# Kernel optimization log

Hardware: AMD Instinct MI355X
Metric: run time of the kernel (lower is better)

Reference implementation:

```python
import jax, jax.numpy as jnp
import numpy as np

B, S, HID = 1, 2048, 2048
NH, NKV, D = 32, 4, 128   # query heads, kv heads, head_dim
ROPE_THETA = 1e6
EPS = 1e-6


def _rms_norm(x, w):
    # per-head RMSNorm over head_dim, computed in fp32 (Qwen3MoeRMSNorm)
    xf = x.astype(jnp.float32)
    var = jnp.mean(xf * xf, axis=-1, keepdims=True)
    return (w * (xf * jax.lax.rsqrt(var + EPS))).astype(x.dtype)


def _rotate_half(x):
    x1, x2 = jnp.split(x, 2, axis=-1)
    return jnp.concatenate([-x2, x1], axis=-1)


def setup_inputs() -> dict:
    key = jax.random.key(0)
    ks = jax.random.split(key, 5)
    hidden_states = jax.random.normal(ks[0], (B, S, HID), jnp.float32)
    # weights stored as (in, out); torch Linear computes x @ W.T with W (out,in) -- same math
    wq = jax.random.normal(ks[1], (HID, NH * D), jnp.float32) * 0.02
    wk = jax.random.normal(ks[2], (HID, NKV * D), jnp.float32) * 0.02
    wv = jax.random.normal(ks[3], (HID, NKV * D), jnp.float32) * 0.02
    wo = jax.random.normal(ks[4], (NH * D, HID), jnp.float32) * 0.02
    q_norm_w = jnp.ones((D,), jnp.float32)
    k_norm_w = jnp.ones((D,), jnp.float32)
    # RoPE tables (rotate_half convention, like HF Qwen3)
    inv_freq = 1.0 / (ROPE_THETA ** (jnp.arange(0, D, 2, dtype=jnp.float32) / D))
    freqs = jnp.arange(S, dtype=jnp.float32)[:, None] * inv_freq[None, :]  # [S, D/2]
    emb = jnp.concatenate([freqs, freqs], axis=-1)  # [S, D]
    cos, sin = jnp.cos(emb), jnp.sin(emb)
    # causal mask (True = keep)
    attention_mask = jnp.tril(jnp.ones((S, S), bool))[None, None]
    return {
        'hidden_states': hidden_states, 'cos': cos, 'sin': sin,
        'wq': wq, 'wk': wk, 'wv': wv, 'wo': wo,
        'q_norm_w': q_norm_w, 'k_norm_w': k_norm_w,
        'attention_mask': attention_mask, 'start_pos': 0,
    }


def reference(hidden_states, cos, sin, wq, wk, wv, wo, q_norm_w, k_norm_w,
              attention_mask, start_pos):
    b, s, _ = hidden_states.shape
    # projections + per-head RMSNorm, then [B, H, S, D]
    q = _rms_norm((hidden_states @ wq).reshape(b, s, NH, D), q_norm_w).transpose(0, 2, 1, 3)
    k = _rms_norm((hidden_states @ wk).reshape(b, s, NKV, D), k_norm_w).transpose(0, 2, 1, 3)
    v = (hidden_states @ wv).reshape(b, s, NKV, D).transpose(0, 2, 1, 3)
    # rotary embedding (rotate_half form); start_pos=0 -> tables already aligned
    c = cos[None, None, :, :]
    sn = sin[None, None, :, :]
    q = q * c + _rotate_half(q) * sn
    k = k * c + _rotate_half(k) * sn
    # GQA: repeat kv heads to match query heads
    groups = NH // NKV
    k = jnp.repeat(k, groups, axis=1)
    v = jnp.repeat(v, groups, axis=1)
    scaling = D ** -0.5
    scores = jnp.einsum('bhqd,bhkd->bhqk', q, k) * scaling  # [B, NH, S, S]
    scores = jnp.where(attention_mask, scores, jnp.float32(-1e9))
    attn = jax.nn.softmax(scores, axis=-1)
    out = jnp.einsum('bhqk,bhkd->bhqd', attn, v)  # [B, NH, S, D]
    out = out.transpose(0, 2, 1, 3).reshape(b, s, NH * D)
    return out @ wo
```

## Files before the change

### kernel.cpp

```cpp
#include <hip/hip_runtime.h>
#include <hip/hip_bf16.h>

using short4v = __attribute__((ext_vector_type(4))) short;
using short8 = __attribute__((ext_vector_type(8))) short;
using f32x4  = __attribute__((ext_vector_type(4))) float;

#define SEQ 2048
#define NHEAD 32
#define NKVH 4
#define HDIM 128
#define QK_SCALE_LOG2 (0.08838834764831845f * 1.44269504088896340f)

__device__ __forceinline__ float fast_exp2(float x) { return __builtin_amdgcn_exp2f(x); }
__device__ __forceinline__ float b2f(short u) {
    return __uint_as_float(((unsigned)(unsigned short)u) << 16);
}
__device__ __forceinline__ short f2bb(float f) {
    __hip_bfloat16 h = __float2bfloat16(f);
    return *reinterpret_cast<short*>(&h);
}

__global__ __launch_bounds__(256) void prep_kernel(
    const float* __restrict__ hs, __hip_bfloat16* __restrict__ hsb,
    const float* __restrict__ wq, const float* __restrict__ wk, const float* __restrict__ wv,
    const float* __restrict__ wo,
    __hip_bfloat16* __restrict__ WqkvT, __hip_bfloat16* __restrict__ WoT) {
    const int b = blockIdx.x, tid = threadIdx.x;
    if (b < 4096) {
        int i = b * 256 + tid;
        float4 v = ((const float4*)hs)[i];
        __hip_bfloat16 h4[4] = {__float2bfloat16(v.x), __float2bfloat16(v.y),
                                __float2bfloat16(v.z), __float2bfloat16(v.w)};
        ((ushort4*)hsb)[i] = *(ushort4*)h4;
        return;
    }
    __shared__ float tile[32][33];
    const float* W; __hip_bfloat16* Wt; int N, ld, nb, kb;
    if (b < 12288)      { int bb = b - 4096;  W = wq; Wt = WqkvT;                       N = 4096; ld = 2048; nb = (bb & 127) * 32; kb = (bb >> 7) * 32; }
    else if (b < 13312) { int bb = b - 12288; W = wk; Wt = WqkvT + (size_t)4096 * 2048; N = 512;  ld = 2048; nb = (bb & 15) * 32;  kb = (bb >> 4) * 32; }
    else if (b < 14336) { int bb = b - 13312; W = wv; Wt = WqkvT + (size_t)4608 * 2048; N = 512;  ld = 2048; nb = (bb & 15) * 32;  kb = (bb >> 4) * 32; }
    else                { int bb = b - 14336; W = wo; Wt = WoT;                         N = 2048; ld = 4096; nb = (bb & 63) * 32;  kb = (bb >> 6) * 32; }
    int tx = tid & 31, ty = tid >> 5;
    for (int j = 0; j < 32; j += 8)
        tile[ty + j][tx] = W[(size_t)(kb + ty + j) * N + nb + tx];
    __syncthreads();
    for (int j = 0; j < 32; j += 8)
        Wt[(size_t)(nb + ty + j) * ld + kb + tx] = __float2bfloat16(tile[tx][ty + j]);
}

__global__ void add3b_kernel(const __hip_bfloat16* __restrict__ a, const __hip_bfloat16* __restrict__ b,
                             const __hip_bfloat16* __restrict__ c, float* __restrict__ o, int n4) {
    int i = blockIdx.x * blockDim.x + threadIdx.x;
    if (i >= n4) return;
    short4v x = ((const short4v*)a)[i];
    short4v y = ((const short4v*)b)[i];
    short4v z = ((const short4v*)c)[i];
    float4 r = {b2f(x[0]) + b2f(y[0]) + b2f(z[0]), b2f(x[1]) + b2f(y[1]) + b2f(z[1]),
                b2f(x[2]) + b2f(y[2]) + b2f(z[2]), b2f(x[3]) + b2f(y[3]) + b2f(z[3])};
    ((float4*)o)[i] = r;
}

#define BM 128
#define BN 128
#define BKK 32
template <typename OutT>
__global__ __launch_bounds__(256) void gemm_bt_kernel(
    const __hip_bfloat16* __restrict__ A, const __hip_bfloat16* __restrict__ Bt,
    OutT* __restrict__ C, int M, int N, int KextMax, int ld, int koff, long long czstride, int Ktot) {
    const int kstart = blockIdx.z * koff;
    const int Kext = min(KextMax, Ktot - kstart);
    A  += (size_t)kstart;
    Bt += (size_t)kstart;
    C  += (size_t)blockIdx.z * czstride;
    __shared__ __align__(16) __hip_bfloat16 sA[BM * BKK];
    __shared__ __align__(16) __hip_bfloat16 sB[BN * BKK];
    const int tid = threadIdx.x;
    const int w = tid >> 6, l = tid & 63;
    const int wr = w >> 1, wc = w & 1;
    const int row0 = blockIdx.y * BM;
    const int col0 = blockIdx.x * BN;
    const int srow = l >> 2;
    const int scol = (l & 3) * 8;

    f32x4 acc[4][4] = {};
    const int fr = l & 15;
    const int fc = (l >> 4) * 8;

    for (int k0 = 0; k0 < Kext; k0 += BKK) {
        for (int i = 0; i < 2; ++i) {
            int c = i * 4 + w;
            const __hip_bfloat16* ga = A + (size_t)(row0 + c * 16 + srow) * ld + k0 + scol;
            __builtin_amdgcn_global_load_lds((const __attribute__((address_space(1))) void*)ga,
                                             (__attribute__((address_space(3))) void*)&sA[c * 16 * BKK], 16, 0, 0);
            const __hip_bfloat16* gb = Bt + (size_t)(col0 + c * 16 + srow) * ld + k0 + scol;
            __builtin_amdgcn_global_load_lds((const __attribute__((address_space(1))) void*)gb,
                                             (__attribute__((address_space(3))) void*)&sB[c * 16 * BKK], 16, 0, 0);
        }
        __syncthreads();
        short8 af[4], bfr[4];
        for (int m = 0; m < 4; ++m)
            af[m] = *(const short8*)&sA[(wr * 64 + m * 16 + fr) * BKK + fc];
        for (int n = 0; n < 4; ++n)
            bfr[n] = *(const short8*)&sB[(wc * 64 + n * 16 + fr) * BKK + fc];
        for (int m = 0; m < 4; ++m)
            for (int n = 0; n < 4; ++n)
                acc[m][n] = __builtin_amdgcn_mfma_f32_16x16x32_bf16(af[m], bfr[n], acc[m][n], 0, 0, 0);
        __syncthreads();
    }
    const int fq = l >> 4;
    for (int m = 0; m < 4; ++m)
        for (int n = 0; n < 4; ++n)
            for (int r = 0; r < 4; ++r) {
                int row = row0 + wr * 64 + m * 16 + fq * 4 + r;
                int col = col0 + wc * 64 + n * 16 + fr;
                float v = acc[m][n][r];
                if constexpr (__is_same(OutT, float)) C[(size_t)row * N + col] = v;
                else C[(size_t)row * N + col] = __float2bfloat16(v);
            }
}

__global__ __launch_bounds__(256) void pack_kernel(
    const __hip_bfloat16* __restrict__ P0, const __hip_bfloat16* __restrict__ P1,
    const float* __restrict__ cosp, const float* __restrict__ sinp,
    const float* __restrict__ qnw, const float* __restrict__ knw,
    __hip_bfloat16* __restrict__ Qh, __hip_bfloat16* __restrict__ Kh, __hip_bfloat16* __restrict__ Vt) {
    const int tid = threadIdx.x;
    const int rloc = tid >> 4, l16 = tid & 15;
    const int r = blockIdx.y * 16 + rloc;
    const int s = blockIdx.x * 2 + (r >= 40 ? 1 : 0);
    const int slot = (r >= 40) ? r - 40 : r;
    int off;
    if (slot < 32)      off = slot * 128;
    else if (slot < 36) off = 4096 + (slot - 32) * 128;
    else                off = 4608 + (slot - 36) * 128;
    const int d0 = l16 * 4;
    const size_t base = (size_t)s * 5120 + off;

    short4v a0 = *(const short4v*)&P0[base + d0];
    short4v a1 = *(const short4v*)&P0[base + d0 + 64];
    short4v b0 = *(const short4v*)&P1[base + d0];
    short4v b1 = *(const short4v*)&P1[base + d0 + 64];
    float x1[4], x2[4];
    for (int j = 0; j < 4; ++j) {
        x1[j] = b2f(a0[j]) + b2f(b0[j]);
        x2[j] = b2f(a1[j]) + b2f(b1[j]);
    }

    if (slot >= 36) {
        int t = slot - 36;
        for (int j = 0; j < 4; ++j) {
            Vt[((size_t)t * 128 + d0 + j) * SEQ + s]      = __float2bfloat16(x1[j]);
            Vt[((size_t)t * 128 + d0 + 64 + j) * SEQ + s] = __float2bfloat16(x2[j]);
        }
        return;
    }
    float ss = 0.f;
    for (int j = 0; j < 4; ++j) ss += x1[j] * x1[j] + x2[j] * x2[j];
    for (int x = 1; x < 16; x <<= 1) ss += __shfl_xor(ss, x);
    float rs = rsqrtf(ss * (1.0f / 128.0f) + 1e-6f);

    f32x4 c4 = *(const f32x4*)&cosp[(size_t)s * 128 + d0];
    f32x4 s4 = *(const f32x4*)&sinp[(size_t)s * 128 + d0];
    const float* wgt = (slot < 32) ? qnw : knw;
    f32x4 w1 = *(const f32x4*)&wgt[d0];
    f32x4 w2 = *(const f32x4*)&wgt[d0 + 64];
    const float scl = (slot < 32) ? QK_SCALE_LOG2 : 1.0f;

    short4v o1, o2;
    for (int j = 0; j < 4; ++j) {
        float a = x1[j] * rs * w1[j], b = x2[j] * rs * w2[j];
        o1[j] = f2bb((a * c4[j] - b * s4[j]) * scl);
        o2[j] = f2bb((b * c4[j] + a * s4[j]) * scl);
    }
    __hip_bfloat16* dst;
    if (slot < 32) dst = Qh + ((size_t)slot * SEQ + s) * 128;
    else           dst = Kh + ((size_t)(slot - 32) * SEQ + s) * 128;
    *(short4v*)&dst[d0]      = o1;
    *(short4v*)&dst[d0 + 64] = o2;
}

__global__ __launch_bounds__(256, 2) void attn_kernel(
    const __hip_bfloat16* __restrict__ Qh,
    const __hip_bfloat16* __restrict__ Kh,
    const __hip_bfloat16* __restrict__ Vt,
    __hip_bfloat16* __restrict__ Oa) {
    __shared__ __align__(16) __hip_bfloat16 sK[2][64 * 128];
    __shared__ __align__(16) __hip_bfloat16 sV[2][128 * 64];
    __shared__ __align__(16) __hip_bfloat16 sP[4][16 * 72];

    const int tid = threadIdx.x;
    const int w = tid >> 6, l = tid & 63;
    const int bx = blockIdx.x;
    const int y = bx & 7;
    const int qt = 127 - (bx >> 3);
    const int qbase = qt * 16;
    const int hkv = y >> 1;
    const int h = y * 4 + w;
    const int fr = l & 15, g = l >> 4;

    const __hip_bfloat16* Qp = Qh + ((size_t)h * SEQ + qbase) * HDIM;
    const __hip_bfloat16* Kp = Kh + (size_t)hkv * SEQ * HDIM;
    const __hip_bfloat16* Vp = Vt + (size_t)hkv * HDIM * SEQ;
    __hip_bfloat16* myP = &sP[w][0];

    short8 qf[4];
    for (int c = 0; c < 4; ++c)
        qf[c] = *(const short8*)&Qp[fr * HDIM + c * 32 + g * 8];

    f32x4 oacc[8] = {};
    float m_s = -3.0e38f;
    float l_s = 0.f;

    const int xr = (fr & 7) << 4;
    const int qg = qbase + fr;
    const int ntiles = ((qbase + 15) >> 6) + 1;

    auto stage = [&](int buf, int kbase) {
        for (int i = 0; i < 4; ++i) {
            int blk = i * 4 + w;
            {
                int row = blk * 4 + (l >> 4);
                int cb = ((l & 15) * 16) ^ ((row & 7) << 4);
                const __hip_bfloat16* src = Kp + (size_t)(kbase + row) * HDIM + (cb >> 1);
                __builtin_amdgcn_global_load_lds((const __attribute__((address_space(1))) void*)src,
                    (__attribute__((address_space(3))) void*)&sK[buf][blk * 512], 16, 0, 0);
            }
            {
                int row = blk * 8 + (l >> 3);
                int cb = ((l & 7) * 16) ^ ((row & 7) << 4);
                const __hip_bfloat16* src = Vp + (size_t)row * SEQ + kbase + (cb >> 1);
                __builtin_amdgcn_global_load_lds((const __attribute__((address_space(1))) void*)src,
                    (__attribute__((address_space(3))) void*)&sV[buf][blk * 512], 16, 0, 0);
            }
        }
    };

    stage(0, 0);
    __syncthreads();

    for (int t = 0; t < ntiles; ++t) {
        const int kbase = t * 64;
        const int buf = t & 1;
        if (t + 1 < ntiles) stage(buf ^ 1, kbase + 64);

        f32x4 s[4] = {};
        __builtin_amdgcn_s_setprio(1);
        for (int j = 0; j < 4; ++j) {
            const __hip_bfloat16* kp = &sK[buf][(j * 16 + fr) * 128];
            for (int c = 0; c < 4; ++c) {
                short8 kf = *(const short8*)&kp[((c * 64 + g * 16) ^ xr) >> 1];
                s[j] = __builtin_amdgcn_mfma_f32_16x16x32_bf16(kf, qf[c], s[j], 0, 0, 0);
            }
        }
        __builtin_amdgcn_s_setprio(0);

        float v[4][4];
        const bool full = (kbase + 63 <= qbase);
        if (full) {
            for (int j = 0; j < 4; ++j)
                for (int r = 0; r < 4; ++r) v[j][r] = s[j][r];
        } else {
            const int kb0 = kbase + g * 4;
            for (int j = 0; j < 4; ++j)
                for (int r = 0; r < 4; ++r)
                    v[j][r] = (kb0 + j * 16 + r <= qg) ? s[j][r] : -1e30f;
        }
        float m0 = fmaxf(fmaxf(v[0][0], v[0][1]), fmaxf(v[0][2], v[0][3]));
        float m1 = fmaxf(fmaxf(v[1][0], v[1][1]), fmaxf(v[1][2], v[1][3]));
        float m2 = fmaxf(fmaxf(v[2][0], v[2][1]), fmaxf(v[2][2], v[2][3]));
        float m3 = fmaxf(fmaxf(v[3][0], v[3][1]), fmaxf(v[3][2], v[3][3]));
        float m = fmaxf(fmaxf(m0, m1), fmaxf(m2, m3));
        m = fmaxf(m, __shfl_xor(m, 16));
        m = fmaxf(m, __shfl_xor(m, 32));
        if (__any(m > m_s + 12.0f)) {
            float mnew = fmaxf(m_s, m);
            float corr = fast_exp2(m_s - mnew);
            m_s = mnew;
            l_s *= corr;
            float c0 = __shfl(corr, g * 4 + 0);
            float c1 = __shfl(corr, g * 4 + 1);
            float c2 = __shfl(corr, g * 4 + 2);
            float c3 = __shfl(corr, g * 4 + 3);
            for (int dt = 0; dt < 8; ++dt) {
                oacc[dt][0] *= c0; oacc[dt][1] *= c1;
                oacc[dt][2] *= c2; oacc[dt][3] *= c3;
            }
        }
        for (int j = 0; j < 4; ++j) {
            float e0 = fast_exp2(v[j][0] - m_s);
            float e1 = fast_exp2(v[j][1] - m_s);
            float e2 = fast_exp2(v[j][2] - m_s);
            float e3 = fast_exp2(v[j][3] - m_s);
            l_s += (e0 + e1) + (e2 + e3);
            short4v pw = {f2bb(e0), f2bb(e1), f2bb(e2), f2bb(e3)};
            *(short4v*)((char*)myP + fr * 144 + j * 32 + g * 8) = pw;
        }
        short8 pa0 = *(const short8*)&myP[fr * 72 + g * 8];
        short8 pa1 = *(const short8*)&myP[fr * 72 + 32 + g * 8];
        __builtin_amdgcn_s_setprio(1);
        for (int dt = 0; dt < 8; ++dt) {
            const __hip_bfloat16* vp = &sV[buf][(dt * 16 + fr) * 64];
            short8 vb0 = *(const short8*)&vp[((g * 16)      ^ xr) >> 1];
            short8 vb1 = *(const short8*)&vp[((g * 16 + 64) ^ xr) >> 1];
            oacc[dt] = __builtin_amdgcn_mfma_f32_16x16x32_bf16(pa0, vb0, oacc[dt], 0, 0, 0);
            oacc[dt] = __builtin_amdgcn_mfma_f32_16x16x32_bf16(pa1, vb1, oacc[dt], 0, 0, 0);
        }
        __builtin_amdgcn_s_setprio(0);
        __syncthreads();
    }

    l_s += __shfl_xor(l_s, 16);
    l_s += __shfl_xor(l_s, 32);
    float inv[4];
    for (int r = 0; r < 4; ++r)
        inv[r] = 1.0f / __shfl(l_s, g * 4 + r);
    for (int dt = 0; dt < 8; ++dt)
        for (int r = 0; r < 4; ++r) {
            int qq = qbase + g * 4 + r;
            Oa[(size_t)qq * (NHEAD * HDIM) + h * HDIM + dt * 16 + fr] =
                __float2bfloat16(oacc[dt][r] * inv[r]);
        }
}

extern "C" void kernel_launch(void* const* d_in, const int* in_sizes, int n_in,
                              void* d_out, int out_size, void* d_ws, size_t ws_size,
                              hipStream_t stream) {
    const float* hs   = (const float*)d_in[0];
    const float* cosp = (const float*)d_in[1];
    const float* sinp = (const float*)d_in[2];
    const float* wq   = (const float*)d_in[3];
    const float* wk   = (const float*)d_in[4];
    const float* wv   = (const float*)d_in[5];
    const float* wo   = (const float*)d_in[6];
    const float* qnw  = (const float*)d_in[7];
    const float* knw  = (const float*)d_in[8];
    float* out = (float*)d_out;
    char* ws = (char*)d_ws;

    __hip_bfloat16* hsb    = (__hip_bfloat16*)(ws);
    __hip_bfloat16* WqkvT  = (__hip_bfloat16*)(ws + 8388608);
    __hip_bfloat16* WoT    = (__hip_bfloat16*)(ws + 29360128);
    __hip_bfloat16* P0     = (__hip_bfloat16*)(ws + 46137344);
    __hip_bfloat16* P1     = (__hip_bfloat16*)(ws + 67108864);
    __hip_bfloat16* Qh     = (__hip_bfloat16*)(ws + 8388608);
    __hip_bfloat16* Kh     = (__hip_bfloat16*)(ws + 25165824);
    __hip_bfloat16* Vt     = (__hip_bfloat16*)(ws + 27262976);
    __hip_bfloat16* Oa     = (__hip_bfloat16*)(ws + 46137344);
    __hip_bfloat16* Qb     = (__hip_bfloat16*)(ws);

    prep_kernel<<<22528, 256, 0, stream>>>(hs, hsb, wq, wk, wv, wo, WqkvT, WoT);
    gemm_bt_kernel<__hip_bfloat16><<<dim3(40, 16, 2), 256, 0, stream>>>(
        hsb, WqkvT, P0, 2048, 5120, 1024, 2048, 1024, 10485760LL, 2048);
    pack_kernel<<<dim3(1024, 5), 256, 0, stream>>>(P0, P1, cosp, sinp, qnw, knw, Qh, Kh, Vt);
    attn_kernel<<<dim3(1024), 256, 0, stream>>>(Qh, Kh, Vt, Oa);
    gemm_bt_kernel<__hip_bfloat16><<<dim3(16, 16, 3), 256, 0, stream>>>(
        Oa, WoT, Qb, 2048, 2048, 1376, 4096, 1376, 4194304LL, 4096);
    add3b_kernel<<<4096, 256, 0, stream>>>(Qb, Qb + 4194304, Qb + 8388608, out, (2048 * 2048) / 4);
}
```

Baseline: 223.4 us.

## Fuse QKV projection GEMM with RMSNorm, RoPE and V transpose epilogue

Replaces the split-K QKV GEMM (two partial outputs) plus a separate pack kernel with one GEMM whose 128-column tile covers a whole head. Per-head RMSNorm, RoPE and scaling are applied in the epilogue, and V is transposed through LDS with coalesced stores. This removes the partial-sum round trip through memory, one kernel launch, and the strided V stores. The cost is dropping split-K, so the grid is 640 blocks of full-K work instead of 1280, which may reduce parallelism on the GEMM.

```diff
diff --git a/kernel.cpp b/kernel.cpp
--- a/kernel.cpp
+++ b/kernel.cpp
@@ -18,6 +18,10 @@
 __device__ __forceinline__ short f2bb(float f) {
     __hip_bfloat16 h = __float2bfloat16(f);
     return *reinterpret_cast<short*>(&h);
+}
+__device__ __forceinline__ void gload_lds16(const __hip_bfloat16* src, __hip_bfloat16* dst) {
+    __builtin_amdgcn_global_load_lds((const __attribute__((address_space(1))) void*)src,
+                                     (__attribute__((address_space(3))) void*)dst, 16, 0, 0);
 }
 
 __global__ __launch_bounds__(256) void prep_kernel(
@@ -89,12 +93,8 @@
     for (int k0 = 0; k0 < Kext; k0 += BKK) {
         for (int i = 0; i < 2; ++i) {
             int c = i * 4 + w;
-            const __hip_bfloat16* ga = A + (size_t)(row0 + c * 16 + srow) * ld + k0 + scol;
-            __builtin_amdgcn_global_load_lds((const __attribute__((address_space(1))) void*)ga,
-                                             (__attribute__((address_space(3))) void*)&sA[c * 16 * BKK], 16, 0, 0);
-            const __hip_bfloat16* gb = Bt + (size_t)(col0 + c * 16 + srow) * ld + k0 + scol;
-            __builtin_amdgcn_global_load_lds((const __attribute__((address_space(1))) void*)gb,
-                                             (__attribute__((address_space(3))) void*)&sB[c * 16 * BKK], 16, 0, 0);
+            gload_lds16(A + (size_t)(row0 + c * 16 + srow) * ld + k0 + scol, &sA[c * 16 * BKK]);
+            gload_lds16(Bt + (size_t)(col0 + c * 16 + srow) * ld + k0 + scol, &sB[c * 16 * BKK]);
         }
         __syncthreads();
         short8 af[4], bfr[4];
@@ -119,64 +119,99 @@
             }
 }
 
-__global__ __launch_bounds__(256) void pack_kernel(
-    const __hip_bfloat16* __restrict__ P0, const __hip_bfloat16* __restrict__ P1,
+__global__ __launch_bounds__(256) void gemm_qkv_fused_kernel(
+    const __hip_bfloat16* __restrict__ A,
+    const __hip_bfloat16* __restrict__ Bt,
     const float* __restrict__ cosp, const float* __restrict__ sinp,
     const float* __restrict__ qnw, const float* __restrict__ knw,
-    __hip_bfloat16* __restrict__ Qh, __hip_bfloat16* __restrict__ Kh, __hip_bfloat16* __restrict__ Vt) {
+    __hip_bfloat16* __restrict__ Qh, __hip_bfloat16* __restrict__ Kh,
+    __hip_bfloat16* __restrict__ Vt) {
+    __shared__ __align__(16) char pool[128 * 136 * 2];
+    __hip_bfloat16* sA    = (__hip_bfloat16*)pool;
+    __hip_bfloat16* sB    = (__hip_bfloat16*)(pool + 8192);
+    __hip_bfloat16* stage = (__hip_bfloat16*)pool;
+
     const int tid = threadIdx.x;
-    const int rloc = tid >> 4, l16 = tid & 15;
-    const int r = blockIdx.y * 16 + rloc;
-    const int s = blockIdx.x * 2 + (r >= 40 ? 1 : 0);
-    const int slot = (r >= 40) ? r - 40 : r;
-    int off;
-    if (slot < 32)      off = slot * 128;
-    else if (slot < 36) off = 4096 + (slot - 32) * 128;
-    else                off = 4608 + (slot - 36) * 128;
-    const int d0 = l16 * 4;
-    const size_t base = (size_t)s * 5120 + off;
-
-    short4v a0 = *(const short4v*)&P0[base + d0];
-    short4v a1 = *(const short4v*)&P0[base + d0 + 64];
-    short4v b0 = *(const short4v*)&P1[base + d0];
-    short4v b1 = *(const short4v*)&P1[base + d0 + 64];
-    float x1[4], x2[4];
-    for (int j = 0; j < 4; ++j) {
-        x1[j] = b2f(a0[j]) + b2f(b0[j]);
-        x2[j] = b2f(a1[j]) + b2f(b1[j]);
-    }
-
-    if (slot >= 36) {
-        int t = slot - 36;
-        for (int j = 0; j < 4; ++j) {
-            Vt[((size_t)t * 128 + d0 + j) * SEQ + s]      = __float2bfloat16(x1[j]);
-            Vt[((size_t)t * 128 + d0 + 64 + j) * SEQ + s] = __float2bfloat16(x2[j]);
-        }
-        return;
-    }
-    float ss = 0.f;
-    for (int j = 0; j < 4; ++j) ss += x1[j] * x1[j] + x2[j] * x2[j];
-    for (int x = 1; x < 16; x <<= 1) ss += __shfl_xor(ss, x);
-    float rs = rsqrtf(ss * (1.0f / 128.0f) + 1e-6f);
-
-    f32x4 c4 = *(const f32x4*)&cosp[(size_t)s * 128 + d0];
-    f32x4 s4 = *(const f32x4*)&sinp[(size_t)s * 128 + d0];
-    const float* wgt = (slot < 32) ? qnw : knw;
-    f32x4 w1 = *(const f32x4*)&wgt[d0];
-    f32x4 w2 = *(const f32x4*)&wgt[d0 + 64];
-    const float scl = (slot < 32) ? QK_SCALE_LOG2 : 1.0f;
-
-    short4v o1, o2;
-    for (int j = 0; j < 4; ++j) {
-        float a = x1[j] * rs * w1[j], b = x2[j] * rs * w2[j];
-        o1[j] = f2bb((a * c4[j] - b * s4[j]) * scl);
-        o2[j] = f2bb((b * c4[j] + a * s4[j]) * scl);
-    }
-    __hip_bfloat16* dst;
-    if (slot < 32) dst = Qh + ((size_t)slot * SEQ + s) * 128;
-    else           dst = Kh + ((size_t)(slot - 32) * SEQ + s) * 128;
-    *(short4v*)&dst[d0]      = o1;
-    *(short4v*)&dst[d0 + 64] = o2;
+    const int w = tid >> 6, l = tid & 63;
+    const int slot = blockIdx.x;
+    const int row0 = blockIdx.y * 128;
+    const int col0 = slot * 128;
+    const int srow = l >> 2, scol = (l & 3) * 8;
+    const int fr = l & 15, fq = l >> 4;
+    const int fc = fq * 8;
+
+    f32x4 acc[2][8] = {};
+    for (int k0 = 0; k0 < 2048; k0 += BKK) {
+        for (int i = 0; i < 2; ++i) {
+            int c = i * 4 + w;
+            gload_lds16(A + (size_t)(row0 + c * 16 + srow) * 2048 + k0 + scol, &sA[c * 16 * BKK]);
+            gload_lds16(Bt + (size_t)(col0 + c * 16 + srow) * 2048 + k0 + scol, &sB[c * 16 * BKK]);
+        }
+        __syncthreads();
+        short8 af[2], bf8[8];
+        for (int m = 0; m < 2; ++m)
+            af[m] = *(const short8*)&sA[(w * 32 + m * 16 + fr) * BKK + fc];
+        for (int n = 0; n < 8; ++n)
+            bf8[n] = *(const short8*)&sB[(n * 16 + fr) * BKK + fc];
+        for (int m = 0; m < 2; ++m)
+            for (int n = 0; n < 8; ++n)
+                acc[m][n] = __builtin_amdgcn_mfma_f32_16x16x32_bf16(af[m], bf8[n], acc[m][n], 0, 0, 0);
+        __syncthreads();
+    }
+
+    if (slot < 36) {
+        const float* wgt = (slot < 32) ? qnw : knw;
+        const float scl = (slot < 32) ? QK_SCALE_LOG2 : 1.0f;
+        float ssq[2][4];
+        for (int m = 0; m < 2; ++m)
+            for (int r = 0; r < 4; ++r) {
+                float s2 = 0.f;
+                for (int n = 0; n < 8; ++n) { float x = acc[m][n][r]; s2 += x * x; }
+                ssq[m][r] = s2;
+            }
+        for (int x = 1; x < 16; x <<= 1)
+            for (int m = 0; m < 2; ++m)
+                for (int r = 0; r < 4; ++r)
+                    ssq[m][r] += __shfl_xor(ssq[m][r], x);
+        float w1[4], w2[4];
+        for (int n = 0; n < 4; ++n) {
+            w1[n] = wgt[n * 16 + fr];
+            w2[n] = wgt[64 + n * 16 + fr];
+        }
+        for (int m = 0; m < 2; ++m)
+            for (int r = 0; r < 4; ++r) {
+                const int row = w * 32 + m * 16 + fq * 4 + r;
+                const int s = row0 + row;
+                const float rs = rsqrtf(ssq[m][r] * (1.0f / 128.0f) + 1e-6f);
+                for (int n = 0; n < 4; ++n) {
+                    float c  = cosp[(size_t)s * 128 + n * 16 + fr];
+                    float sn = sinp[(size_t)s * 128 + n * 16 + fr];
+                    float a = acc[m][n][r] * rs * w1[n];
+                    float b = acc[m][n + 4][r] * rs * w2[n];
+                    stage[row * 136 + n * 16 + fr]      = __float2bfloat16((a * c - b * sn) * scl);
+                    stage[row * 136 + 64 + n * 16 + fr] = __float2bfloat16((b * c + a * sn) * scl);
+                }
+            }
+        __syncthreads();
+        const int rr = tid >> 1, hf = tid & 1;
+        __hip_bfloat16* dst = (slot < 32)
+            ? Qh + ((size_t)slot * SEQ + row0 + rr) * 128 + hf * 64
+            : Kh + ((size_t)(slot - 32) * SEQ + row0 + rr) * 128 + hf * 64;
+        for (int j = 0; j < 8; ++j)
+            *(short8*)&dst[j * 8] = *(const short8*)&stage[rr * 136 + hf * 64 + j * 8];
+    } else {
+        for (int m = 0; m < 2; ++m)
+            for (int r = 0; r < 4; ++r) {
+                const int row = w * 32 + m * 16 + fq * 4 + r;
+                for (int n = 0; n < 8; ++n)
+                    stage[(n * 16 + fr) * 136 + row] = __float2bfloat16(acc[m][n][r]);
+            }
+        __syncthreads();
+        const int d = tid >> 1, sh = tid & 1;
+        __hip_bfloat16* dst = Vt + ((size_t)(slot - 36) * 128 + d) * SEQ + row0 + sh * 64;
+        for (int j = 0; j < 8; ++j)
+            *(short8*)&dst[j * 8] = *(const short8*)&stage[d * 136 + sh * 64 + j * 8];
+    }
 }
 
 __global__ __launch_bounds__(256, 2) void attn_kernel(
@@ -221,16 +256,12 @@
             {
                 int row = blk * 4 + (l >> 4);
                 int cb = ((l & 15) * 16) ^ ((row & 7) << 4);
-                const __hip_bfloat16* src = Kp + (size_t)(kbase + row) * HDIM + (cb >> 1);
-                __builtin_amdgcn_global_load_lds((const __attribute__((address_space(1))) void*)src,
-                    (__attribute__((address_space(3))) void*)&sK[buf][blk * 512], 16, 0, 0);
+                gload_lds16(Kp + (size_t)(kbase + row) * HDIM + (cb >> 1), &sK[buf][blk * 512]);
             }
             {
                 int row = blk * 8 + (l >> 3);
                 int cb = ((l & 7) * 16) ^ ((row & 7) << 4);
-                const __hip_bfloat16* src = Vp + (size_t)row * SEQ + kbase + (cb >> 1);
-                __builtin_amdgcn_global_load_lds((const __attribute__((address_space(1))) void*)src,
-                    (__attribute__((address_space(3))) void*)&sV[buf][blk * 512], 16, 0, 0);
+                gload_lds16(Vp + (size_t)row * SEQ + kbase + (cb >> 1), &sV[buf][blk * 512]);
             }
         }
     };
@@ -340,18 +371,15 @@
     __hip_bfloat16* hsb    = (__hip_bfloat16*)(ws);
     __hip_bfloat16* WqkvT  = (__hip_bfloat16*)(ws + 8388608);
     __hip_bfloat16* WoT    = (__hip_bfloat16*)(ws + 29360128);
-    __hip_bfloat16* P0     = (__hip_bfloat16*)(ws + 46137344);
-    __hip_bfloat16* P1     = (__hip_bfloat16*)(ws + 67108864);
-    __hip_bfloat16* Qh     = (__hip_bfloat16*)(ws + 8388608);
-    __hip_bfloat16* Kh     = (__hip_bfloat16*)(ws + 25165824);
-    __hip_bfloat16* Vt     = (__hip_bfloat16*)(ws + 27262976);
-    __hip_bfloat16* Oa     = (__hip_bfloat16*)(ws + 46137344);
-    __hip_bfloat16* Qb     = (__hip_bfloat16*)(ws);
+    __hip_bfloat16* Qh     = (__hip_bfloat16*)(ws + 46137344);
+    __hip_bfloat16* Kh     = (__hip_bfloat16*)(ws + 62914560);
+    __hip_bfloat16* Vt     = (__hip_bfloat16*)(ws + 65011712);
+    __hip_bfloat16* Oa     = (__hip_bfloat16*)(ws + 8388608);
+    __hip_bfloat16* Qb     = (__hip_bfloat16*)(ws + 46137344);
 
     prep_kernel<<<22528, 256, 0, stream>>>(hs, hsb, wq, wk, wv, wo, WqkvT, WoT);
-    gemm_bt_kernel<__hip_bfloat16><<<dim3(40, 16, 2), 256, 0, stream>>>(
-        hsb, WqkvT, P0, 2048, 5120, 1024, 2048, 1024, 10485760LL, 2048);
-    pack_kernel<<<dim3(1024, 5), 256, 0, stream>>>(P0, P1, cosp, sinp, qnw, knw, Qh, Kh, Vt);
+    gemm_qkv_fused_kernel<<<dim3(40, 16), 256, 0, stream>>>(
+        hsb, WqkvT, cosp, sinp, qnw, knw, Qh, Kh, Vt);
     attn_kernel<<<dim3(1024), 256, 0, stream>>>(Qh, Kh, Vt, Oa);
     gemm_bt_kernel<__hip_bfloat16><<<dim3(16, 16, 3), 256, 0, stream>>>(
         Oa, WoT, Qb, 2048, 2048, 1376, 4096, 1376, 4194304LL, 4096);
```

New measurement: 234.9 us. 5.2% more time.
